# Optimization experiments

Measured on AMD Instinct MI355X. Metric: run time of the kernel, lower is better.

Reference implementation:

```python
import jax, jax.numpy as jnp
import numpy as np

N_SRC = 100000
N_DST = 50000
N_EDGES = 1000000
D = 64
N_CLASSES = 64


def setup_inputs() -> dict:
    key = jax.random.key(0)
    ks = jax.random.split(key, 6)
    x = jax.random.normal(ks[0], (N_SRC, D), dtype=jnp.float32)
    w = jax.random.uniform(ks[1], (N_EDGES,), dtype=jnp.float32)
    u_sum = jax.random.uniform(ks[2], (N_SRC,), dtype=jnp.float32)
    W_w = jax.random.normal(ks[3], (N_CLASSES, 2 * D), dtype=jnp.float32) * (1.0 / np.sqrt(2 * D))
    W_b = jax.random.normal(ks[4], (N_CLASSES,), dtype=jnp.float32) * 0.01
    src_idx = jax.random.randint(ks[5], (N_EDGES,), 0, N_SRC, dtype=jnp.int64 if jax.config.jax_enable_x64 else jnp.int32)
    dst_idx = jax.random.randint(jax.random.fold_in(key, 7), (N_EDGES,), 0, N_DST, dtype=jnp.int64 if jax.config.jax_enable_x64 else jnp.int32)
    return {"x": x, "w": w, "u_sum": u_sum, "W_w": W_w, "W_b": W_b,
            "src_idx": src_idx, "dst_idx": dst_idx, "n_dst": N_DST}


def reference(x, w, u_sum, W_w, W_b, src_idx, dst_idx, n_dst):
    n_src, d = x.shape
    out_dim = W_w.shape[0]
    x_dst = x[:n_dst]                                  # dstdata['x']
    msgs = x[src_idx]                                  # [E, d] gather (u)
    # First update_all: u_mul_e + sum. NOTE: in the original module this result
    # is immediately overwritten by the second update_all, so it is dead math;
    # computed here for structural fidelity (XLA will DCE it).
    y_wsum = jax.ops.segment_sum(msgs * w[:, None], dst_idx, num_segments=n_dst)
    # Second update_all: copy_u + mean -> this is the 'y' actually used.
    deg = jax.ops.segment_sum(jnp.ones_like(w), dst_idx, num_segments=n_dst)
    y_mean = jax.ops.segment_sum(msgs, dst_idx, num_segments=n_dst) / jnp.maximum(deg, 1.0)[:, None]
    h = jnp.concatenate([x_dst, y_mean], axis=1) @ W_w.T + W_b  # [n_dst, out_dim]
    mean_x = jnp.mean(y_mean, axis=0)                  # [d]
    mean_u = u_sum / n_dst                             # [n_src]
    diff = mean_u[:, None] * x - mean_x                # [n_src, d]
    reg_loss = jnp.sum(diff * diff) / (n_src * out_dim)
    return h, reg_loss
```

## Files before the change

### kernel.cpp

```cpp
#include <hip/hip_runtime.h>

#define N_SRC   100000
#define N_DSTC  50000
#define N_EDGES 1000000
#define DIM     64
#define NCLS    64

#define SCAN_BPB 256
#define SCAN_NB  ((N_DSTC + SCAN_BPB - 1) / SCAN_BPB)

#define HIST_BLOCKS ((N_EDGES / 4 + 255) / 256)
#define REG_BLOCKS  1024
#define GATHER_GRID 1024


__global__ __launch_bounds__(256) void hist_reg_kernel(
    const int4*  __restrict__ dst4,
    const float* __restrict__ x,
    const float* __restrict__ u_sum,
    int*   __restrict__ hist,
    float* __restrict__ regA,
    float* __restrict__ regB) {
  __shared__ float redB[4][64];
  __shared__ float redA[4];

  if (blockIdx.x < HIST_BLOCKS) {
    int i = blockIdx.x * blockDim.x + threadIdx.x;
    if (i < N_EDGES / 4) {
      int4 d = dst4[i];
      atomicAdd(&hist[d.x], 1);
      atomicAdd(&hist[d.y], 1);
      atomicAdd(&hist[d.z], 1);
      atomicAdd(&hist[d.w], 1);
    }
    return;
  }

  const int tid  = threadIdx.x;
  const int wv   = tid >> 6;
  const int lane = tid & 63;
  const int waveId     = (blockIdx.x - HIST_BLOCKS) * 4 + wv;
  const int totalWaves = REG_BLOCKS * 4;

  float accA = 0.0f;
  float accB = 0.0f;
  for (int r = waveId; r < N_SRC; r += totalWaves) {
    float u  = u_sum[r];
    float xv = x[r * DIM + lane];
    float t  = u * xv;
    accB += t;
    accA = fmaf(t, t, accA);
  }
  #pragma unroll
  for (int off = 32; off > 0; off >>= 1)
    accA += __shfl_down(accA, off, 64);
  if (lane == 0) redA[wv] = accA;
  redB[wv][lane] = accB;
  __syncthreads();
  if (tid < 64) {
    float b = redB[0][tid] + redB[1][tid] + redB[2][tid] + redB[3][tid];
    atomicAdd(&regB[tid], b);
  }
  if (tid == 0) {
    float a = redA[0] + redA[1] + redA[2] + redA[3];
    atomicAdd(regA, a);
  }
}

__global__ __launch_bounds__(256) void scan_local(
    const int* __restrict__ hist, int* __restrict__ cursor,
    int* __restrict__ blockSums) {
  __shared__ int A[256], B[256];
  const int b = blockIdx.x, t = threadIdx.x;
  const int g = b * SCAN_BPB + t;
  int v = (g < N_DSTC) ? hist[g] : 0;
  A[t] = v;
  __syncthreads();
  int* cur = A; int* nxt = B;
  for (int off = 1; off < 256; off <<= 1) {
    int s = cur[t] + ((t >= off) ? cur[t - off] : 0);
    nxt[t] = s;
    __syncthreads();
    int* tmp = cur; cur = nxt; nxt = tmp;
  }
  if (g < N_DSTC) cursor[g] = cur[t] - v;
  if (t == 255) blockSums[b] = cur[255];
}

__global__ __launch_bounds__(256) void scan_addoff(
    int* __restrict__ cursor, const int* __restrict__ blockSums) {
  __shared__ int A[256], B[256];
  const int b = blockIdx.x, t = threadIdx.x;
  A[t] = (t < SCAN_NB) ? blockSums[t] : 0;
  __syncthreads();
  int* cur = A; int* nxt = B;
  for (int off = 1; off < 256; off <<= 1) {
    int s = cur[t] + ((t >= off) ? cur[t - off] : 0);
    nxt[t] = s;
    __syncthreads();
    int* tmp = cur; cur = nxt; nxt = tmp;
  }
  int off = (b > 0) ? cur[b - 1] : 0;
  int g = b * SCAN_BPB + t;
  if (g < N_DSTC) cursor[g] += off;
}

__global__ __launch_bounds__(256) void reorder_kernel(
    const int4* __restrict__ src4, const int4* __restrict__ dst4,
    int* __restrict__ cursor, int* __restrict__ sorted_src) {
  int i = blockIdx.x * blockDim.x + threadIdx.x;
  if (i < N_EDGES / 4) {
    int4 s = src4[i];
    int4 d = dst4[i];
    int p0 = atomicAdd(&cursor[d.x], 1); sorted_src[p0] = s.x;
    int p1 = atomicAdd(&cursor[d.y], 1); sorted_src[p1] = s.y;
    int p2 = atomicAdd(&cursor[d.z], 1); sorted_src[p2] = s.z;
    int p3 = atomicAdd(&cursor[d.w], 1); sorted_src[p3] = s.w;
  }
}

__global__ __launch_bounds__(256, 4) void gather_h(
    const float* __restrict__ x,
    const float* __restrict__ Ww,
    const float* __restrict__ Wb,
    const int*   __restrict__ cursor,
    const int*   __restrict__ sorted_src,
    float* __restrict__ h,
    float* __restrict__ colsum,
    float* __restrict__ regA,
    float* __restrict__ regB,
    int*   __restrict__ doneG,
    float* __restrict__ out_scalar) {
  __shared__ float Wt[2 * DIM][NCLS + 1];
  __shared__ float colred[4][64];
  __shared__ int   lastFlag;

  const int tid = threadIdx.x;
  for (int idx = tid; idx < NCLS * 2 * DIM; idx += 256) {
    int c = idx >> 7, k = idx & 127;
    Wt[k][c] = Ww[idx];
  }
  __syncthreads();

  const int wv   = tid >> 6;
  const int lane = tid & 63;
  const int es   = lane >> 4;
  const int q    = lane & 15;
  const int waveId = blockIdx.x * 4 + wv;
  const int tw     = gridDim.x * 4;
  const float bias = Wb[lane];
  const float4* x4 = reinterpret_cast<const float4*>(x);

  float4 colacc = make_float4(0.f, 0.f, 0.f, 0.f);

  for (int r = waveId; r < N_DSTC; r += tw) {
    int beg = (r == 0) ? 0 : cursor[r - 1];
    int end = cursor[r];
    int cnt = end - beg;

    float4 a = make_float4(0.f, 0.f, 0.f, 0.f);
    for (int base = 0; base < cnt; base += 64) {
      int rem = cnt - base;
      int mm  = rem < 64 ? rem : 64;
      int idxv = (lane < rem) ? sorted_src[beg + base + lane] : 0;

      int jb = 0;
      for (; jb + 8 <= mm; jb += 8) {
        int s0 = __shfl(idxv, jb + es,     64);
        int s1 = __shfl(idxv, jb + 4 + es, 64);
        float4 v0 = x4[s0 * 16 + q];
        float4 v1 = x4[s1 * 16 + q];
        a.x += v0.x + v1.x;
        a.y += v0.y + v1.y;
        a.z += v0.z + v1.z;
        a.w += v0.w + v1.w;
      }
      for (; jb < mm; jb += 4) {
        int j = jb + es;
        int s0 = __shfl(idxv, j & 63, 64);
        if (j < mm) {
          float4 v = x4[s0 * 16 + q];
          a.x += v.x; a.y += v.y; a.z += v.z; a.w += v.w;
        }
      }
    }
    a.x += __shfl_xor(a.x, 16, 64); a.y += __shfl_xor(a.y, 16, 64);
    a.z += __shfl_xor(a.z, 16, 64); a.w += __shfl_xor(a.w, 16, 64);
    a.x += __shfl_xor(a.x, 32, 64); a.y += __shfl_xor(a.y, 32, 64);
    a.z += __shfl_xor(a.z, 32, 64); a.w += __shfl_xor(a.w, 32, 64);

    float inv = 1.0f / fmaxf((float)cnt, 1.0f);
    float4 ym = make_float4(a.x * inv, a.y * inv, a.z * inv, a.w * inv);

    float4 xv = x4[r * 16 + q];

    if (es == 0) {
      colacc.x += ym.x; colacc.y += ym.y; colacc.z += ym.z; colacc.w += ym.w;
    }

    float hacc = bias;
    #pragma unroll
    for (int k = 0; k < DIM; ++k) {
      const int sl = k >> 2;
      float fx = __shfl((k & 3) == 0 ? xv.x : (k & 3) == 1 ? xv.y :
                        (k & 3) == 2 ? xv.z : xv.w, sl, 64);
      float fy = __shfl((k & 3) == 0 ? ym.x : (k & 3) == 1 ? ym.y :
                        (k & 3) == 2 ? ym.z : ym.w, sl, 64);
      hacc = fmaf(fx, Wt[k][lane], hacc);
      hacc = fmaf(fy, Wt[DIM + k][lane], hacc);
    }
    h[r * NCLS + lane] = hacc;
  }

  if (es == 0) {
    colred[wv][q * 4 + 0] = colacc.x;
    colred[wv][q * 4 + 1] = colacc.y;
    colred[wv][q * 4 + 2] = colacc.z;
    colred[wv][q * 4 + 3] = colacc.w;
  }
  __syncthreads();
  if (tid < 64) {
    float s = colred[0][tid] + colred[1][tid] + colred[2][tid] + colred[3][tid];
    atomicAdd(&colsum[tid], s);
  }

  __syncthreads();
  if (tid == 0) {
    __threadfence();
    int old = atomicAdd(doneG, 1);
    lastFlag = (old == (int)gridDim.x - 1) ? 1 : 0;
  }
  __syncthreads();
  if (lastFlag && tid < 64) {
    const float inv_nd = 1.0f / (float)N_DSTC;
    float cs = atomicAdd(&colsum[tid], 0.0f);
    float bv = atomicAdd(&regB[tid], 0.0f);
    float mx = cs * inv_nd;
    float p = fmaf((float)N_SRC * mx, mx, -2.0f * inv_nd * mx * bv);
    #pragma unroll
    for (int off = 32; off > 0; off >>= 1)
      p += __shfl_down(p, off, 64);
    if (tid == 0) {
      float av = atomicAdd(regA, 0.0f);
      float total = fmaf(av, inv_nd * inv_nd, p);
      out_scalar[0] = total * (1.0f / ((float)N_SRC * (float)NCLS));
    }
  }
}

extern "C" void kernel_launch(void* const* d_in, const int* in_sizes, int n_in,
                              void* d_out, int out_size, void* d_ws, size_t ws_size,
                              hipStream_t stream) {
  const float* x     = (const float*)d_in[0];
  const float* u_sum = (const float*)d_in[2];
  const float* Ww    = (const float*)d_in[3];
  const float* Wb    = (const float*)d_in[4];
  const int*   src   = (const int*)d_in[5];
  const int*   dst   = (const int*)d_in[6];

  float* out = (float*)d_out;
  int*   wsI = (int*)d_ws;

  int*   hist       = wsI;
  float* colsum     = (float*)(wsI + N_DSTC);
  float* regA       = colsum + 64;
  float* regB       = regA + 1;
  int*   doneG      = (int*)(regB + 64);
  int*   blockSums  = doneG + 1;
  int*   cursor     = blockSums + SCAN_NB;
  int*   sorted_src = cursor + N_DSTC;

  hipMemsetAsync(d_ws, 0, (size_t)(N_DSTC + 64 + 1 + 64 + 1) * sizeof(int), stream);

  hist_reg_kernel<<<HIST_BLOCKS + REG_BLOCKS, 256, 0, stream>>>(
      (const int4*)dst, x, u_sum, hist, regA, regB);
  scan_local  <<<SCAN_NB, 256, 0, stream>>>(hist, cursor, blockSums);
  scan_addoff <<<SCAN_NB, 256, 0, stream>>>(cursor, blockSums);
  reorder_kernel<<<(N_EDGES / 4 + 255) / 256, 256, 0, stream>>>(
      (const int4*)src, (const int4*)dst, cursor, sorted_src);
  gather_h    <<<GATHER_GRID, 256, 0, stream>>>(
      x, Ww, Wb, cursor, sorted_src, out, colsum, regA, regB, doneG,
      out + (size_t)N_DSTC * NCLS);
}
```

Measured before the change: 392.6 us.

## Merge scan into single-block kernel, scalarize reorder, simplify gather loop, double grid

Replaces the two-pass multi-block scan with one 1024-thread block in which each thread serially sums and writes a chunk of about 49 entries. The reorder kernel now handles one edge per thread instead of four via int4 loads. The gather inner loop loses its two-loads-per-iteration unroll, uses 64-bit indexing, and drops the occupancy hint, while the gather grid doubles. Together these trade one kernel launch for a serial, uncoalesced single-block scan and reduce per-thread memory-level parallelism in the gather.

```diff
diff --git a/kernel.cpp b/kernel.cpp
--- a/kernel.cpp
+++ b/kernel.cpp
@@ -6,12 +6,9 @@
 #define DIM     64
 #define NCLS    64
 
-#define SCAN_BPB 256
-#define SCAN_NB  ((N_DSTC + SCAN_BPB - 1) / SCAN_BPB)
-
 #define HIST_BLOCKS ((N_EDGES / 4 + 255) / 256)
 #define REG_BLOCKS  1024
-#define GATHER_GRID 1024
+#define GATHER_GRID 2048
 
 
 __global__ __launch_bounds__(256) void hist_reg_kernel(
@@ -67,59 +64,46 @@
   }
 }
 
-__global__ __launch_bounds__(256) void scan_local(
-    const int* __restrict__ hist, int* __restrict__ cursor,
-    int* __restrict__ blockSums) {
-  __shared__ int A[256], B[256];
-  const int b = blockIdx.x, t = threadIdx.x;
-  const int g = b * SCAN_BPB + t;
-  int v = (g < N_DSTC) ? hist[g] : 0;
-  A[t] = v;
-  __syncthreads();
-  int* cur = A; int* nxt = B;
-  for (int off = 1; off < 256; off <<= 1) {
-    int s = cur[t] + ((t >= off) ? cur[t - off] : 0);
-    nxt[t] = s;
+__global__ __launch_bounds__(1024) void scan_kernel(
+    const int* __restrict__ hist, int* __restrict__ cursor) {
+  __shared__ int bufA[1024];
+  __shared__ int bufB[1024];
+  const int t = threadIdx.x;
+  const int chunk = (N_DSTC + 1023) / 1024;
+  int beg = t * chunk;       if (beg > N_DSTC) beg = N_DSTC;
+  int end = beg + chunk;     if (end > N_DSTC) end = N_DSTC;
+
+  int s = 0;
+  for (int i = beg; i < end; ++i) s += hist[i];
+  bufA[t] = s;
+  __syncthreads();
+
+  int* cur = bufA;
+  int* nxt = bufB;
+  for (int off = 1; off < 1024; off <<= 1) {
+    int v = cur[t] + ((t >= off) ? cur[t - off] : 0);
+    nxt[t] = v;
     __syncthreads();
     int* tmp = cur; cur = nxt; nxt = tmp;
   }
-  if (g < N_DSTC) cursor[g] = cur[t] - v;
-  if (t == 255) blockSums[b] = cur[255];
-}
-
-__global__ __launch_bounds__(256) void scan_addoff(
-    int* __restrict__ cursor, const int* __restrict__ blockSums) {
-  __shared__ int A[256], B[256];
-  const int b = blockIdx.x, t = threadIdx.x;
-  A[t] = (t < SCAN_NB) ? blockSums[t] : 0;
-  __syncthreads();
-  int* cur = A; int* nxt = B;
-  for (int off = 1; off < 256; off <<= 1) {
-    int s = cur[t] + ((t >= off) ? cur[t - off] : 0);
-    nxt[t] = s;
-    __syncthreads();
-    int* tmp = cur; cur = nxt; nxt = tmp;
-  }
-  int off = (b > 0) ? cur[b - 1] : 0;
-  int g = b * SCAN_BPB + t;
-  if (g < N_DSTC) cursor[g] += off;
+  int run = (t > 0) ? cur[t - 1] : 0;
+  for (int i = beg; i < end; ++i) {
+    cursor[i] = run;
+    run += hist[i];
+  }
 }
 
 __global__ __launch_bounds__(256) void reorder_kernel(
-    const int4* __restrict__ src4, const int4* __restrict__ dst4,
+    const int* __restrict__ src, const int* __restrict__ dst,
     int* __restrict__ cursor, int* __restrict__ sorted_src) {
-  int i = blockIdx.x * blockDim.x + threadIdx.x;
-  if (i < N_EDGES / 4) {
-    int4 s = src4[i];
-    int4 d = dst4[i];
-    int p0 = atomicAdd(&cursor[d.x], 1); sorted_src[p0] = s.x;
-    int p1 = atomicAdd(&cursor[d.y], 1); sorted_src[p1] = s.y;
-    int p2 = atomicAdd(&cursor[d.z], 1); sorted_src[p2] = s.z;
-    int p3 = atomicAdd(&cursor[d.w], 1); sorted_src[p3] = s.w;
-  }
-}
-
-__global__ __launch_bounds__(256, 4) void gather_h(
+  int e = blockIdx.x * blockDim.x + threadIdx.x;
+  if (e < N_EDGES) {
+    int pos = atomicAdd(&cursor[dst[e]], 1);
+    sorted_src[pos] = src[e];
+  }
+}
+
+__global__ __launch_bounds__(256) void gather_h(
     const float* __restrict__ x,
     const float* __restrict__ Ww,
     const float* __restrict__ Wb,
@@ -163,23 +147,12 @@
       int rem = cnt - base;
       int mm  = rem < 64 ? rem : 64;
       int idxv = (lane < rem) ? sorted_src[beg + base + lane] : 0;
-
-      int jb = 0;
-      for (; jb + 8 <= mm; jb += 8) {
-        int s0 = __shfl(idxv, jb + es,     64);
-        int s1 = __shfl(idxv, jb + 4 + es, 64);
-        float4 v0 = x4[s0 * 16 + q];
-        float4 v1 = x4[s1 * 16 + q];
-        a.x += v0.x + v1.x;
-        a.y += v0.y + v1.y;
-        a.z += v0.z + v1.z;
-        a.w += v0.w + v1.w;
-      }
-      for (; jb < mm; jb += 4) {
-        int j = jb + es;
-        int s0 = __shfl(idxv, j & 63, 64);
+      int nIt = (mm + 3) >> 2;
+      for (int jj = 0; jj < nIt; ++jj) {
+        int j = (jj << 2) + es;
+        int sIdx = __shfl(idxv, j & 63, 64);
         if (j < mm) {
-          float4 v = x4[s0 * 16 + q];
+          float4 v = x4[(long long)sIdx * 16 + q];
           a.x += v.x; a.y += v.y; a.z += v.z; a.w += v.w;
         }
       }
@@ -192,7 +165,7 @@
     float inv = 1.0f / fmaxf((float)cnt, 1.0f);
     float4 ym = make_float4(a.x * inv, a.y * inv, a.z * inv, a.w * inv);
 
-    float4 xv = x4[r * 16 + q];
+    float4 xv = x4[(long long)r * 16 + q];
 
     if (es == 0) {
       colacc.x += ym.x; colacc.y += ym.y; colacc.z += ym.z; colacc.w += ym.w;
@@ -209,7 +182,7 @@
       hacc = fmaf(fx, Wt[k][lane], hacc);
       hacc = fmaf(fy, Wt[DIM + k][lane], hacc);
     }
-    h[r * NCLS + lane] = hacc;
+    h[(long long)r * NCLS + lane] = hacc;
   }
 
   if (es == 0) {
@@ -266,19 +239,17 @@
   float* regA       = colsum + 64;
   float* regB       = regA + 1;
   int*   doneG      = (int*)(regB + 64);
-  int*   blockSums  = doneG + 1;
-  int*   cursor     = blockSums + SCAN_NB;
+  int*   cursor     = doneG + 1;
   int*   sorted_src = cursor + N_DSTC;
 
   hipMemsetAsync(d_ws, 0, (size_t)(N_DSTC + 64 + 1 + 64 + 1) * sizeof(int), stream);
 
   hist_reg_kernel<<<HIST_BLOCKS + REG_BLOCKS, 256, 0, stream>>>(
       (const int4*)dst, x, u_sum, hist, regA, regB);
-  scan_local  <<<SCAN_NB, 256, 0, stream>>>(hist, cursor, blockSums);
-  scan_addoff <<<SCAN_NB, 256, 0, stream>>>(cursor, blockSums);
-  reorder_kernel<<<(N_EDGES / 4 + 255) / 256, 256, 0, stream>>>(
-      (const int4*)src, (const int4*)dst, cursor, sorted_src);
-  gather_h    <<<GATHER_GRID, 256, 0, stream>>>(
+  scan_kernel   <<<1, 1024, 0, stream>>>(hist, cursor);
+  reorder_kernel<<<(N_EDGES + 255) / 256, 256, 0, stream>>>(
+      src, dst, cursor, sorted_src);
+  gather_h      <<<GATHER_GRID, 256, 0, stream>>>(
       x, Ww, Wb, cursor, sorted_src, out, colsum, regA, regB, doneG,
       out + (size_t)N_DSTC * NCLS);
 }
```

New measurement: 463.0 us. +17.9%, slower.
